# Kernel tuning notes

Hardware: AMD Instinct MI355X
Metric: run time of the kernel (lower is better)

The kernel has to match this reference:

```python
import jax, jax.numpy as jnp
import numpy as np
from jax import lax


def conv2d(x, w, pad=0, b=None):
    out = lax.conv_general_dilated(x, w, (1, 1), [(pad, pad), (pad, pad)],
                                   dimension_numbers=('NCHW', 'OIHW', 'NCHW'))
    if b is not None:
        out = out + b[None, :, None, None]
    return out


def bilinear_resize(x, hw):
    # matches F.interpolate(mode='bilinear', align_corners=False) (half-pixel centers)
    return jax.image.resize(x, x.shape[:2] + tuple(hw), method='bilinear')


def dcn_v2(x, off_feat, w_om, b_om, w, b, dg=8):
    # modulated deformable conv v2, kernel 3x3, stride 1, pad 1, dilation 1
    om = conv2d(off_feat, w_om, pad=1, b=b_om)          # [B, 3*dg*9, H, W]
    B, C, H, W = x.shape
    KK = 9
    Cpg = C // dg
    o1, o2, m = jnp.split(om, 3, axis=1)
    off_y = o1.reshape(B, dg, KK, H, W)
    off_x = o2.reshape(B, dg, KK, H, W)
    mask = jax.nn.sigmoid(m).reshape(B, dg, KK, H, W)
    ks = jnp.arange(3, dtype=x.dtype) - 1.0
    ky = jnp.repeat(ks, 3)   # [9] kernel row offsets
    kx = jnp.tile(ks, 3)     # [9] kernel col offsets
    gy = jnp.arange(H, dtype=x.dtype)
    gx = jnp.arange(W, dtype=x.dtype)
    # sampling coords [B, dg, 9, H, W]
    y = gy[None, None, None, :, None] + ky[None, None, :, None, None] + off_y
    xx = gx[None, None, None, None, :] + kx[None, None, :, None, None] + off_x
    y0 = jnp.floor(y)
    x0 = jnp.floor(xx)
    xg = x.reshape(B, dg, Cpg, H * W)
    val = jnp.zeros((B, dg, Cpg, KK, H, W), x.dtype)
    for dy in (0.0, 1.0):
        for dx in (0.0, 1.0):
            yi = y0 + dy
            xi = x0 + dx
            wgt = (1.0 - jnp.abs(y - yi)) * (1.0 - jnp.abs(xx - xi))
            valid = (yi >= 0) & (yi < H) & (xi >= 0) & (xi < W)  # zero padding outside
            idx = (jnp.clip(yi, 0, H - 1) * W + jnp.clip(xi, 0, W - 1)).astype(jnp.int32)
            idxf = idx.reshape(B, dg, 1, KK * H * W)
            g = jnp.take_along_axis(xg, jnp.broadcast_to(idxf, (B, dg, Cpg, KK * H * W)), axis=3)
            val = val + g.reshape(B, dg, Cpg, KK, H, W) * (wgt * valid)[:, :, None]
    val = val * mask[:, :, None]                         # modulation
    Cout = w.shape[0]
    out = jnp.einsum('bgckhw,ogck->bohw', val, w.reshape(Cout, dg, Cpg, KK))
    return out + b[None, :, None, None]


def sem(x, w_sa, bn_g, bn_b, bn_m, bn_v, w1, gn_g, gn_b):
    # spatial attention
    avg = jnp.mean(x, axis=1, keepdims=True)
    mx = jnp.max(x, axis=1, keepdims=True)
    a = conv2d(jnp.concatenate([avg, mx], axis=1), w_sa, pad=3)
    a = (a - bn_m[None, :, None, None]) * lax.rsqrt(bn_v + 1e-5)[None, :, None, None]
    a = a * bn_g[None, :, None, None] + bn_b[None, :, None, None]
    sa = jax.nn.sigmoid(a)
    x = x + x * sa
    y = conv2d(x, w1)
    # GroupNorm, 32 groups
    B, C, H, W = y.shape
    G = 32
    yr = y.reshape(B, G, C // G, H, W)
    mu = jnp.mean(yr, axis=(2, 3, 4), keepdims=True)
    var = jnp.var(yr, axis=(2, 3, 4), keepdims=True)
    yn = ((yr - mu) * lax.rsqrt(var + 1e-5)).reshape(B, C, H, W)
    return yn * gn_g[None, :, None, None] + gn_b[None, :, None, None]


def setup_inputs() -> dict:
    key = jax.random.key(0)
    ks = jax.random.split(key, 16)
    B, C = 4, 256
    f32 = jnp.float32
    inp = {
        'feat_l': jax.random.normal(ks[0], (B, C, 128, 128), f32),
        'feat_3': jax.random.normal(ks[1], (B, C, 64, 64), f32),
        'feat_4': jax.random.normal(ks[2], (B, C, 32, 32), f32),
        'feat_5': jax.random.normal(ks[3], (B, C, 16, 16), f32),
        'w_off5': jax.random.normal(ks[4], (256, 512, 1, 1), f32) * 0.05,
        'w_om5': jax.random.normal(ks[5], (216, 256, 3, 3), f32) * 0.01,
        'b_om5': jnp.zeros((216,), f32),
        'w_dcn5': jax.random.normal(ks[6], (256, 256, 3, 3), f32) * 0.05,
        'b_dcn5': jnp.zeros((256,), f32),
        'w_c1': jax.random.normal(ks[7], (256, 512, 1, 1), f32) * 0.05,
        'w_off4': jax.random.normal(ks[8], (256, 512, 1, 1), f32) * 0.05,
        'w_om4': jax.random.normal(ks[9], (216, 256, 3, 3), f32) * 0.01,
        'b_om4': jnp.zeros((216,), f32),
        'w_dcn4': jax.random.normal(ks[10], (256, 256, 3, 3), f32) * 0.05,
        'b_dcn4': jnp.zeros((256,), f32),
        'w_sa': jax.random.normal(ks[11], (1, 2, 7, 7), f32) * 0.05,
        'bn_g': jnp.ones((1,), f32),
        'bn_b': jnp.zeros((1,), f32),
        'bn_m': jnp.zeros((1,), f32),
        'bn_v': jnp.ones((1,), f32),
        'w_sem': jax.random.normal(ks[12], (256, 512, 1, 1), f32) * 0.05,
        'gn_g': jnp.ones((256,), f32),
        'gn_b': jnp.zeros((256,), f32),
    }
    return inp


def reference(feat_l, feat_3, feat_4, feat_5,
              w_off5, w_om5, b_om5, w_dcn5, b_dcn5, w_c1,
              w_off4, w_om4, b_om4, w_dcn4, b_dcn4,
              w_sa, bn_g, bn_b, bn_m, bn_v, w_sem, gn_g, gn_b):
    HW4 = feat_4.shape[2:]
    feat_up5 = bilinear_resize(feat_5, HW4)
    off5 = conv2d(jnp.concatenate([feat_4, feat_up5 * 2.0], axis=1), w_off5)
    feat_5_align = jax.nn.relu(dcn_v2(feat_up5, off5, w_om5, b_om5, w_dcn5, b_dcn5))
    feat_4 = conv2d(jnp.concatenate([feat_5_align, feat_4], axis=1), w_c1)
    HW3 = feat_3.shape[2:]
    feat_up4 = bilinear_resize(feat_4, HW3)
    off4 = conv2d(jnp.concatenate([feat_3, feat_up4 * 2.0], axis=1), w_off4)
    feat_4_align = jax.nn.relu(dcn_v2(feat_up4, off4, w_om4, b_om4, w_dcn4, b_dcn4))
    feat_3 = jnp.concatenate([feat_4_align, feat_3], axis=1)
    HW2 = feat_l.shape[2:]
    feat_2 = bilinear_resize(feat_3, HW2)
    return sem(feat_2, w_sa, bn_g, bn_b, bn_m, bn_v, w_sem, gn_g, gn_b)
```

## Files before the change

### kernel.cpp

```cpp
#include <hip/hip_runtime.h>
#include <math.h>


typedef _Float16 h_t;
typedef _Float16 h2 __attribute__((ext_vector_type(2)));
typedef _Float16 h4 __attribute__((ext_vector_type(4)));
typedef _Float16 h8 __attribute__((ext_vector_type(8)));
typedef float f4 __attribute__((ext_vector_type(4)));

static inline int cdiv(long long a, long long b) { return (int)((a + b - 1) / b); }

template <int PERM>
__global__ void prep_w_kernel(const float* __restrict__ W, h_t* __restrict__ Wp,
                              int M, int K) {
  long long idx = (long long)blockIdx.x * 256 + threadIdx.x;
  if (idx >= 512LL * K) return;
  int within = (int)(idx & 4095);
  int m = within >> 5, k = within & 31;
  long long t2 = idx >> 12;
  int s = (int)(t2 & 1);
  long long t3 = t2 >> 1;
  int nck = K >> 5;
  int c = (int)(t3 % nck), mblk = (int)(t3 / nck);
  int gm = mblk * 128 + m, gk = c * 32 + k;
  if (PERM) gk = (gk & 255) * 9 + (gk >> 8);
  float f = (gm < M) ? W[(long long)gm * K + gk] : 0.f;
  h_t hi = (h_t)f;
  Wp[idx] = s ? (h_t)(f - (float)hi) : hi;
}

template <int LOGOW>
__global__ void upsample2x_q_kernel(const float* __restrict__ in, float* __restrict__ out,
                                    int NQ) {
  const int OW = 1 << LOGOW, OHW = OW * OW, IW = OW >> 1;
  long long idx = (long long)blockIdx.x * 256 + threadIdx.x;
  if (idx >= (long long)NQ * OHW) return;
  int p = (int)(idx & (OHW - 1));
  int q = (int)(idx >> (2 * LOGOW));
  int oh = p >> LOGOW, ow = p & (OW - 1);
  int iy = oh >> 1, ix = ow >> 1;
  int iy2 = (oh & 1) ? min(iy + 1, IW - 1) : max(iy - 1, 0);
  int ix2 = (ow & 1) ? min(ix + 1, IW - 1) : max(ix - 1, 0);
  const float* pb = in + (long long)q * 4 * IW * IW;
  f4 o;
#pragma unroll
  for (int j = 0; j < 4; ++j) {
    const float* pc = pb + (long long)j * IW * IW;
    o[j] = 0.5625f * pc[iy * IW + ix] + 0.1875f * (pc[iy * IW + ix2] + pc[iy2 * IW + ix])
         + 0.0625f * pc[iy2 * IW + ix2];
  }
  *(f4*)(out + idx * 4) = o;
}

template <typename TA>
__global__ void concat_h_kernel(const TA* __restrict__ A, const float* __restrict__ Bp,
                                h_t* __restrict__ out, int C1, int C2, int HW, float scale) {
  long long idx = (long long)blockIdx.x * blockDim.x + threadIdx.x;
  long long total = 4LL * (C1 + C2) * HW;
  if (idx >= total) return;
  int p = (int)(idx % HW);
  long long t = idx / HW;
  int c = (int)(t % (C1 + C2));
  int b = (int)(t / (C1 + C2));
  float v;
  if (c < C1) v = (float)A[((long long)b * C1 + c) * HW + p];
  else        v = scale * Bp[((long long)b * C2 + (c - C1)) * HW + p];
  out[idx] = (h_t)v;
}

template <typename TA>
__global__ void concat_a_kernel(const TA* __restrict__ A, h_t* __restrict__ out,
                                int C1, int Ctot, int HW) {
  long long idx = (long long)blockIdx.x * 256 + threadIdx.x;
  long long total = 4LL * C1 * HW;
  if (idx >= total) return;
  int p = (int)(idx % HW);
  long long t = idx / HW;
  int c = (int)(t % C1);
  int b = (int)(t / C1);
  out[((long long)b * Ctot + c) * HW + p] = (h_t)(float)A[((long long)b * C1 + c) * HW + p];
}

__global__ void concat_bq_kernel(const float* __restrict__ xq, h_t* __restrict__ out,
                                 int C1, int C2, int HW, float scale) {
  long long idx = (long long)blockIdx.x * 256 + threadIdx.x;
  long long total = 4LL * (C2 >> 2) * HW;
  if (idx >= total) return;
  int p = (int)(idx % HW);
  long long t = idx / HW;
  int q = (int)(t % (C2 >> 2));
  int b = (int)(t / (C2 >> 2));
  f4 v = *(const f4*)(xq + ((long long)(b * (C2 >> 2) + q) * HW + p) * 4);
  h_t* ob = out + ((long long)b * (C1 + C2) + C1 + q * 4) * HW + p;
  ob[0]            = (h_t)(scale * v.x);
  ob[(long long)HW]     = (h_t)(scale * v.y);
  ob[(long long)2 * HW] = (h_t)(scale * v.z);
  ob[(long long)3 * HW] = (h_t)(scale * v.w);
}

template <int RELU, int OUTH, int TWO>
__global__ __launch_bounds__(256) void mgemm_kernel(
    const h_t* __restrict__ Wp, const h_t* __restrict__ B, void* __restrict__ Cv,
    const float* __restrict__ bias, int Mstore, int N, int K,
    long long sB, long long sC) {
  __shared__ __align__(16) h_t Ah[128 * 40];
  __shared__ __align__(16) h_t Al[TWO ? 128 * 40 : 8];
  __shared__ __align__(16) h_t Bs[64 * 40];
  const int tid = threadIdx.x;
  const int bn = blockIdx.x * 64;
  const int mblk = blockIdx.y;
  const int z = blockIdx.z;
  const h_t* Bb = B + (long long)z * sB;
  const int nck = K >> 5;
  const h_t* Wt = Wp + (long long)mblk * nck * 8192 +
                  (TWO ? (tid << 5) : ((tid >> 1) << 5) + ((tid & 1) << 4));
  const int wid = tid >> 6, lane = tid & 63;
  const int wm = (wid >> 1) * 64, wn = (wid & 1) * 32;
  const int l15 = lane & 15, q = lane >> 4;
  f4 acc[4][2] = {};
  h_t* Adst = TWO ? (tid >= 128 ? Al : Ah) + (tid & 127) * 40
                  : Ah + (tid >> 1) * 40 + ((tid & 1) << 4);
  const int kp = tid >> 4, ngf = tid & 15;
  h_t* Bdst = Bs + ngf * 4 * 40 + kp * 2;
  for (int c = 0; c < nck; ++c) {
    const h_t* asrc = Wt + c * 8192;
    if (TWO) {
#pragma unroll
      for (int i = 0; i < 4; ++i)
        *(h8*)(Adst + i * 8) = *(const h8*)(asrc + i * 8);
    } else {
      *(h8*)(Adst) = *(const h8*)(asrc);
      *(h8*)(Adst + 8) = *(const h8*)(asrc + 8);
    }
    const h_t* bsrc = Bb + (long long)(c * 32 + kp * 2) * N + bn + ngf * 4;
    h4 r0 = *(const h4*)bsrc;
    h4 r1 = *(const h4*)(bsrc + N);
#pragma unroll
    for (int j = 0; j < 4; ++j) {
      h2 v; v.x = r0[j]; v.y = r1[j];
      *(h2*)(Bdst + j * 40) = v;
    }
    __syncthreads();
    h8 bf[2];
#pragma unroll
    for (int nt = 0; nt < 2; ++nt)
      bf[nt] = *(const h8*)(Bs + (wn + nt * 16 + l15) * 40 + q * 8);
#pragma unroll
    for (int mt = 0; mt < 4; ++mt) {
      const int ro = (wm + mt * 16 + l15) * 40 + q * 8;
      h8 ahi = *(const h8*)(Ah + ro);
#pragma unroll
      for (int nt = 0; nt < 2; ++nt)
        acc[mt][nt] = __builtin_amdgcn_mfma_f32_16x16x32_f16(ahi, bf[nt], acc[mt][nt], 0, 0, 0);
      if (TWO) {
        h8 alo = *(const h8*)(Al + ro);
#pragma unroll
        for (int nt = 0; nt < 2; ++nt)
          acc[mt][nt] = __builtin_amdgcn_mfma_f32_16x16x32_f16(alo, bf[nt], acc[mt][nt], 0, 0, 0);
      }
    }
    __syncthreads();
  }
#pragma unroll
  for (int mt = 0; mt < 4; ++mt)
#pragma unroll
    for (int nt = 0; nt < 2; ++nt) {
      int n = bn + wn + nt * 16 + l15;
      if (OUTH == 2) {
        int row0 = mblk * 128 + wm + mt * 16 + q * 4;
        if (row0 + 3 < Mstore) {
          h4 hv;
#pragma unroll
          for (int r = 0; r < 4; ++r) {
            float v = acc[mt][nt][r] + (bias ? bias[row0 + r] : 0.f);
            if (RELU) v = fmaxf(v, 0.f);
            hv[r] = (h_t)v;
          }
          *(h4*)((h_t*)Cv + (long long)z * sC + (long long)n * 256 + row0) = hv;
        }
      } else {
#pragma unroll
        for (int r = 0; r < 4; ++r) {
          int row = mblk * 128 + wm + mt * 16 + q * 4 + r;
          if (row < Mstore) {
            float v = acc[mt][nt][r] + (bias ? bias[row] : 0.f);
            if (RELU) v = fmaxf(v, 0.f);
            if (OUTH) ((h_t*)Cv)[(long long)z * sC + (long long)row * N + n] = (h_t)v;
            else      ((float*)Cv)[(long long)z * sC + (long long)row * N + n] = v;
          }
        }
      }
    }
}

template <int LOGW>
__global__ __launch_bounds__(256) void mconv_kernel(
    const h_t* __restrict__ Wp, const h_t* __restrict__ OffT, float* __restrict__ Cf,
    const float* __restrict__ bias, int HW) {
  const int W = 1 << LOGW, H = HW >> LOGW;
  const int tid = threadIdx.x;
  const int p0 = blockIdx.x * 64;
  const int mblk = blockIdx.y;
  const int z = blockIdx.z;
  const h_t* Ot = OffT + (long long)z * HW * 256;
  const h_t* Wb = Wp + (long long)mblk * 72 * 8192;
  const int wid = tid >> 6, lane = tid & 63;
  const int wm = (wid >> 1) * 64, wn = (wid & 1) * 32;
  const int l15 = lane & 15, q = lane >> 4;
  const int aoff = (wm + l15) * 32 + q * 8;
  f4 acc[4][2] = {};
  int py[2], px[2];
#pragma unroll
  for (int nt = 0; nt < 2; ++nt) {
    int p = p0 + wn + nt * 16 + l15;
    py[nt] = p >> LOGW;
    px[nt] = p & (W - 1);
  }
  for (int tap = 0; tap < 9; ++tap) {
    const int dy = tap / 3 - 1, dx = tap - (tap / 3) * 3 - 1;
    const h_t* bsrc[2];
    bool bok[2];
#pragma unroll
    for (int nt = 0; nt < 2; ++nt) {
      int sy = py[nt] + dy, sx = px[nt] + dx;
      bok[nt] = (sy >= 0) & (sy < H) & (sx >= 0) & (sx < W);
      int sp = bok[nt] ? (sy * W + sx) : 0;
      bsrc[nt] = Ot + (long long)sp * 256 + q * 8;
    }
#pragma unroll 2
    for (int c2 = 0; c2 < 8; ++c2) {
      const int c = tap * 8 + c2;
      h8 bf[2];
#pragma unroll
      for (int nt = 0; nt < 2; ++nt) {
        h8 v = {};
        if (bok[nt]) v = *(const h8*)(bsrc[nt] + c2 * 32);
        bf[nt] = v;
      }
      const h_t* aw = Wb + (long long)c * 8192 + aoff;
#pragma unroll
      for (int mt = 0; mt < 4; ++mt) {
        h8 af = *(const h8*)(aw + mt * 512);
#pragma unroll
        for (int nt = 0; nt < 2; ++nt)
          acc[mt][nt] = __builtin_amdgcn_mfma_f32_16x16x32_f16(af, bf[nt], acc[mt][nt], 0, 0, 0);
      }
    }
  }
  float* Cb = Cf + (long long)z * 216 * HW;
#pragma unroll
  for (int mt = 0; mt < 4; ++mt)
#pragma unroll
    for (int nt = 0; nt < 2; ++nt) {
      int n = p0 + wn + nt * 16 + l15;
#pragma unroll
      for (int r = 0; r < 4; ++r) {
        int row = mblk * 128 + wm + mt * 16 + q * 4 + r;
        if (row < 216)
          Cb[(long long)row * HW + n] = acc[mt][nt][r] + bias[row];
      }
    }
}

template <int LOGW>
__global__ __launch_bounds__(256) void dcn_col_kernel(
    const float* __restrict__ x, const float* __restrict__ om,
    h_t* __restrict__ col, int b0) {
  const int W = 1 << LOGW, H = W, HW = W * W;
  int p = blockIdx.x * 256 + threadIdx.x;
  int gk = blockIdx.y;
  int g = gk / 9, k9 = gk - g * 9;
  int bz = blockIdx.z;
  int b = b0 + bz;
  int h = p >> LOGW, wc = p & (W - 1);
  const float* omb = om + (long long)b * 216 * HW;
  float offy = omb[(long long)gk * HW + p];
  float offx = omb[(long long)(72 + gk) * HW + p];
  float mraw = omb[(long long)(144 + gk) * HW + p];
  float mask = 1.f / (1.f + expf(-mraw));
  float y = (float)h + (float)(k9 / 3 - 1) + offy;
  float xx = (float)wc + (float)(k9 % 3 - 1) + offx;
  float y0f = floorf(y), x0f = floorf(xx);
  int y0 = (int)y0f, x0 = (int)x0f;
  float fy = y - y0f, fx = xx - x0f;
  float w00 = (1.f - fy) * (1.f - fx), w01 = (1.f - fy) * fx;
  float w10 = fy * (1.f - fx), w11 = fy * fx;
  bool iy0 = (y0 >= 0) & (y0 < H), iy1 = (y0 + 1 >= 0) & (y0 + 1 < H);
  bool ix0 = (x0 >= 0) & (x0 < W), ix1 = (x0 + 1 >= 0) & (x0 + 1 < W);
  w00 = (iy0 & ix0) ? w00 : 0.f;
  w01 = (iy0 & ix1) ? w01 : 0.f;
  w10 = (iy1 & ix0) ? w10 : 0.f;
  w11 = (iy1 & ix1) ? w11 : 0.f;
  int y0c = min(max(y0, 0), H - 1), y1c = min(max(y0 + 1, 0), H - 1);
  int x0c = min(max(x0, 0), W - 1), x1c = min(max(x0 + 1, 0), W - 1);
  int i00 = y0c * W + x0c, i01 = y0c * W + x1c, i10 = y1c * W + x0c, i11 = y1c * W + x1c;
  const float* xb = x + ((long long)b * 256 + g * 32) * HW;
  h_t* cb = col + ((long long)bz * 2304 + (long long)(g * 32) * 9 + k9) * HW + p;
#pragma unroll 1
  for (int qd = 0; qd < 8; qd += 2) {
    f4 a00[2], a01[2], a10[2], a11[2];
#pragma unroll
    for (int u = 0; u < 2; ++u) {
      const float* xq = xb + (long long)(qd + u) * HW * 4;
      a00[u] = *(const f4*)(xq + i00 * 4);
      a01[u] = *(const f4*)(xq + i01 * 4);
      a10[u] = *(const f4*)(xq + i10 * 4);
      a11[u] = *(const f4*)(xq + i11 * 4);
    }
#pragma unroll
    for (int u = 0; u < 2; ++u)
#pragma unroll
      for (int j = 0; j < 4; ++j) {
        float v = w00 * a00[u][j] + w01 * a01[u][j] + w10 * a10[u][j] + w11 * a11[u][j];
        cb[(long long)((qd + u) * 4 + j) * 9 * HW] = (h_t)(v * mask);
      }
  }
}

__global__ void avgmax_kernel(const h_t* __restrict__ f3c, float* __restrict__ am) {
  int tid = threadIdx.x;
  int P = blockIdx.x * 64 + (tid >> 2);
  int cq = tid & 3;
  int b = P >> 14, p = P & 16383;
  int oh = p >> 7, ow = p & 127;
  int iy = oh >> 1, ix = ow >> 1;
  int iy2 = (oh & 1) ? min(iy + 1, 63) : max(iy - 1, 0);
  int ix2 = (ow & 1) ? min(ix + 1, 63) : max(ix - 1, 0);
  int i00 = iy * 64 + ix, i01 = iy * 64 + ix2, i10 = iy2 * 64 + ix, i11 = iy2 * 64 + ix2;
  const h_t* base = f3c + (long long)b * 512 * 4096 + (long long)cq * 4096;
  float sum = 0.f, mx = -3.4e38f;
  for (int c = 0; c < 128; c++) {
    const h_t* pc = base + (long long)c * 4 * 4096;
    float v = 0.5625f * (float)pc[i00] + 0.1875f * ((float)pc[i01] + (float)pc[i10])
            + 0.0625f * (float)pc[i11];
    sum += v;
    mx = fmaxf(mx, v);
  }
  sum += __shfl_xor(sum, 1); sum += __shfl_xor(sum, 2);
  mx = fmaxf(mx, __shfl_xor(mx, 1)); mx = fmaxf(mx, __shfl_xor(mx, 2));
  if (cq == 0) {
    am[(long long)b * 2 * 16384 + p] = sum * (1.f / 512.f);
    am[(long long)b * 2 * 16384 + 16384 + p] = mx;
  }
}

__global__ void sa_kernel(const float* __restrict__ am, const float* __restrict__ w_sa,
                          const float* __restrict__ bn_g, const float* __restrict__ bn_b,
                          const float* __restrict__ bn_m, const float* __restrict__ bn_v,
                          float* __restrict__ sa) {
  int idx = blockIdx.x * 64 + threadIdx.x;
  int b = idx >> 14, p = idx & 16383;
  int oh = p >> 7, ow = p & 127;
  float acc = 0.f;
  for (int ci = 0; ci < 2; ci++) {
    const float* base = am + ((long long)b * 2 + ci) * 16384;
    for (int dy = 0; dy < 7; dy++) {
      int yy = oh + dy - 3;
      if (yy < 0 || yy > 127) continue;
      for (int dx = 0; dx < 7; dx++) {
        int xx = ow + dx - 3;
        if (xx < 0 || xx > 127) continue;
        acc += w_sa[ci * 49 + dy * 7 + dx] * base[yy * 128 + xx];
      }
    }
  }
  float a = (acc - bn_m[0]) * rsqrtf(bn_v[0] + 1e-5f);
  a = a * bn_g[0] + bn_b[0];
  sa[idx] = 1.f / (1.f + expf(-a));
}

__global__ __launch_bounds__(256) void gn_partials_kernel(
    const float* __restrict__ z, const float* __restrict__ sa,
    float2* __restrict__ partials) {
  long long idx = (long long)blockIdx.x * 256 + threadIdx.x;
  int ow = (int)(idx & 127);
  long long t = idx >> 7;
  int oh = (int)(t & 127);
  t >>= 7;
  int c = (int)(t & 255);
  int b = (int)(t >> 8);
  int iy = oh >> 1, ix = ow >> 1;
  int iy2 = (oh & 1) ? min(iy + 1, 63) : max(iy - 1, 0);
  int ix2 = (ow & 1) ? min(ix + 1, 63) : max(ix - 1, 0);
  const float* zp = z + (long long)(b * 256 + c) * 4096;
  float v = 0.5625f * zp[iy * 64 + ix] + 0.1875f * (zp[iy * 64 + ix2] + zp[iy2 * 64 + ix])
          + 0.0625f * zp[iy2 * 64 + ix2];
  float s = sa[((long long)b << 14) + (oh << 7) + ow];
  float y = v * (1.f + s);
  float ps = y, pss = y * y;
#pragma unroll
  for (int off = 32; off > 0; off >>= 1) {
    ps += __shfl_down(ps, off);
    pss += __shfl_down(pss, off);
  }
  __shared__ float rs[2][4];
  int lane = threadIdx.x & 63, wv = threadIdx.x >> 6;
  if (lane == 0) { rs[0][wv] = ps; rs[1][wv] = pss; }
  __syncthreads();
  if (threadIdx.x == 0) {
    float2 pr;
    pr.x = rs[0][0] + rs[0][1] + rs[0][2] + rs[0][3];
    pr.y = rs[1][0] + rs[1][1] + rs[1][2] + rs[1][3];
    partials[blockIdx.x] = pr;
  }
}

__global__ __launch_bounds__(256) void gn_reduce_kernel(const float2* __restrict__ partials,
                                                        float* __restrict__ stats) {
  int bg = blockIdx.x;
  int b = bg >> 5, g = bg & 31;
  int base = b * 16384 + g * 512;
  float2 p0 = partials[base + threadIdx.x];
  float2 p1 = partials[base + 256 + threadIdx.x];
  float s = p0.x + p1.x, ss = p0.y + p1.y;
#pragma unroll
  for (int off = 32; off > 0; off >>= 1) {
    s += __shfl_down(s, off);
    ss += __shfl_down(ss, off);
  }
  __shared__ float rs[2][4];
  int lane = threadIdx.x & 63, wv = threadIdx.x >> 6;
  if (lane == 0) { rs[0][wv] = s; rs[1][wv] = ss; }
  __syncthreads();
  if (threadIdx.x == 0) {
    float S = rs[0][0] + rs[0][1] + rs[0][2] + rs[0][3];
    float SS = rs[1][0] + rs[1][1] + rs[1][2] + rs[1][3];
    float n = 8.f * 16384.f;
    float mu = S / n;
    float var = SS / n - mu * mu;
    stats[bg * 2] = mu;
    stats[bg * 2 + 1] = rsqrtf(var + 1e-5f);
  }
}

__global__ __launch_bounds__(256) void gn_apply_fused_kernel(
    const float* __restrict__ z, const float* __restrict__ sa,
    const float* __restrict__ stats, const float* __restrict__ gg,
    const float* __restrict__ gb, float* __restrict__ out) {
  long long i4 = (long long)blockIdx.x * 256 + threadIdx.x;
  long long e = i4 << 2;
  int ow0 = (int)(e & 127);
  int oh = (int)((e >> 7) & 127);
  int c = (int)((e >> 14) & 255);
  int b = (int)(e >> 22);
  int bg = b * 32 + (c >> 3);
  float mu = stats[bg * 2], rstd = stats[bg * 2 + 1];
  float sc = rstd * gg[c];
  float sh = gb[c] - mu * sc;
  int iy = oh >> 1;
  int iy2 = (oh & 1) ? min(iy + 1, 63) : max(iy - 1, 0);
  const float* zp = z + (long long)(b * 256 + c) * 4096;
  f4 sv = *(const f4*)(sa + (((long long)b << 14) + (oh << 7) + ow0));
  f4 o;
#pragma unroll
  for (int j = 0; j < 4; ++j) {
    int ow = ow0 + j;
    int ix = ow >> 1;
    int ix2 = (ow & 1) ? min(ix + 1, 63) : max(ix - 1, 0);
    float v = 0.5625f * zp[iy * 64 + ix] + 0.1875f * (zp[iy * 64 + ix2] + zp[iy2 * 64 + ix])
            + 0.0625f * zp[iy2 * 64 + ix2];
    float y = v * (1.f + sv[j]);
    o[j] = y * sc + sh;
  }
  *(f4*)(out + e) = o;
}


extern "C" void kernel_launch(void* const* d_in, const int* in_sizes, int n_in,
                              void* d_out, int out_size, void* d_ws, size_t ws_size,
                              hipStream_t stream) {
  const float* feat_3 = (const float*)d_in[1];
  const float* feat_4 = (const float*)d_in[2];
  const float* feat_5 = (const float*)d_in[3];
  const float* w_off5 = (const float*)d_in[4];
  const float* w_om5  = (const float*)d_in[5];
  const float* b_om5  = (const float*)d_in[6];
  const float* w_dcn5 = (const float*)d_in[7];
  const float* b_dcn5 = (const float*)d_in[8];
  const float* w_c1   = (const float*)d_in[9];
  const float* w_off4 = (const float*)d_in[10];
  const float* w_om4  = (const float*)d_in[11];
  const float* b_om4  = (const float*)d_in[12];
  const float* w_dcn4 = (const float*)d_in[13];
  const float* b_dcn4 = (const float*)d_in[14];
  const float* w_sa   = (const float*)d_in[15];
  const float* bn_g   = (const float*)d_in[16];
  const float* bn_b   = (const float*)d_in[17];
  const float* bn_m   = (const float*)d_in[18];
  const float* bn_v   = (const float*)d_in[19];
  const float* w_sem  = (const float*)d_in[20];
  const float* gn_g   = (const float*)d_in[21];
  const float* gn_b   = (const float*)d_in[22];
  float* out = (float*)d_out;
  float* ws = (float*)d_ws;

  const long long o_Wp    = 0;
  const long long o_up5   = o_Wp + 2883584;
  const long long o_off5h = o_up5 + 1048576;
  const long long o_om5   = o_off5h + 524288;
  const long long o_a5    = o_om5 + 884736;
  const long long o_f4n   = o_a5 + 1048576;
  const long long o_up4   = o_f4n + 1048576;
  const long long o_off4h = o_up4 + 4194304;
  const long long o_om4   = o_off4h + 2097152;
  const long long o_sh    = o_om4 + 3538944;

  const long long shAll = 18874368;
  bool allb = ws_size >= (size_t)(o_sh + shAll) * 4;

  h_t* WpH = (h_t*)ws;
  h_t* wp_off5 = WpH;
  h_t* wp_dcn5 = wp_off5 + 262144;
  h_t* wp_c1   = wp_dcn5 + 1179648;
  h_t* wp_om5  = wp_c1 + 262144;
  h_t* wp_off4 = wp_om5 + 1179648;
  h_t* wp_dcn4 = wp_off4 + 262144;
  h_t* wp_om4  = wp_dcn4 + 1179648;
  h_t* wp_sem  = wp_om4 + 1179648;

  float* up5   = ws + o_up5;
  h_t*   off5h = (h_t*)(ws + o_off5h);
  float* om5   = ws + o_om5;
  float* a5    = ws + o_a5;
  float* f4n   = ws + o_f4n;
  float* up4   = ws + o_up4;
  h_t*   off4h = (h_t*)(ws + o_off4h);
  float* om4   = ws + o_om4;
  h_t*   shH   = (h_t*)(ws + o_sh);
  h_t*   f4aH  = off4h;
  float* z64   = up4;
  float* am    = up5;
  float* sa    = am + 131072;
  float* gnst  = sa + 65536;
  float2* gnpart = (float2*)(gnst + 256);

  dim3 blk(256);

  prep_w_kernel<0><<<cdiv(512LL * 512, 256), blk, 0, stream>>>(w_off5, wp_off5, 256, 512);
  prep_w_kernel<0><<<cdiv(512LL * 2304, 256), blk, 0, stream>>>(w_dcn5, wp_dcn5, 256, 2304);
  prep_w_kernel<0><<<cdiv(512LL * 512, 256), blk, 0, stream>>>(w_c1, wp_c1, 256, 512);
  prep_w_kernel<1><<<cdiv(512LL * 2304, 256), blk, 0, stream>>>(w_om5, wp_om5, 216, 2304);
  prep_w_kernel<0><<<cdiv(512LL * 512, 256), blk, 0, stream>>>(w_off4, wp_off4, 256, 512);
  prep_w_kernel<0><<<cdiv(512LL * 2304, 256), blk, 0, stream>>>(w_dcn4, wp_dcn4, 256, 2304);
  prep_w_kernel<1><<<cdiv(512LL * 2304, 256), blk, 0, stream>>>(w_om4, wp_om4, 216, 2304);
  prep_w_kernel<0><<<cdiv(512LL * 512, 256), blk, 0, stream>>>(w_sem, wp_sem, 256, 512);

  upsample2x_q_kernel<5><<<1024, blk, 0, stream>>>(feat_5, up5, 256);
  concat_a_kernel<float><<<cdiv(4LL * 256 * 1024, 256), blk, 0, stream>>>(
      feat_4, shH, 256, 512, 1024);
  concat_bq_kernel<<<cdiv(4LL * 64 * 1024, 256), blk, 0, stream>>>(
      up5, shH, 256, 256, 1024, 2.f);
  mgemm_kernel<0, 2, 0><<<dim3(16, 2, 4), blk, 0, stream>>>(
      wp_off5, shH, off5h, nullptr, 256, 1024, 512, 512LL * 1024, 256LL * 1024);
  mconv_kernel<5><<<dim3(16, 2, 4), blk, 0, stream>>>(wp_om5, off5h, om5, b_om5, 1024);
  dcn_col_kernel<5><<<dim3(4, 72, 4), blk, 0, stream>>>(up5, om5, shH, 0);
  mgemm_kernel<1, 0, 1><<<dim3(16, 2, 4), blk, 0, stream>>>(
      wp_dcn5, shH, a5, b_dcn5, 256, 1024, 2304, 2304LL * 1024, 256LL * 1024);
  concat_h_kernel<float><<<cdiv(4LL * 512 * 1024, 256), blk, 0, stream>>>(
      a5, feat_4, shH, 256, 256, 1024, 1.f);
  mgemm_kernel<0, 0, 1><<<dim3(16, 2, 4), blk, 0, stream>>>(
      wp_c1, shH, f4n, nullptr, 256, 1024, 512, 512LL * 1024, 256LL * 1024);

  upsample2x_q_kernel<6><<<4096, blk, 0, stream>>>(f4n, up4, 256);
  concat_a_kernel<float><<<cdiv(4LL * 256 * 4096, 256), blk, 0, stream>>>(
      feat_3, shH, 256, 512, 4096);
  concat_bq_kernel<<<cdiv(4LL * 64 * 4096, 256), blk, 0, stream>>>(
      up4, shH, 256, 256, 4096, 2.f);
  mgemm_kernel<0, 2, 0><<<dim3(64, 2, 4), blk, 0, stream>>>(
      wp_off4, shH, off4h, nullptr, 256, 4096, 512, 512LL * 4096, 256LL * 4096);
  mconv_kernel<6><<<dim3(64, 2, 4), blk, 0, stream>>>(wp_om4, off4h, om4, b_om4, 4096);
  if (allb) {
    dcn_col_kernel<6><<<dim3(16, 72, 4), blk, 0, stream>>>(up4, om4, shH, 0);
    mgemm_kernel<1, 1, 1><<<dim3(64, 2, 4), blk, 0, stream>>>(
        wp_dcn4, shH, f4aH, b_dcn4, 256, 4096, 2304, 2304LL * 4096, 256LL * 4096);
  } else {
    for (int b = 0; b < 4; b++) {
      dcn_col_kernel<6><<<dim3(16, 72, 1), blk, 0, stream>>>(up4, om4, shH, b);
      mgemm_kernel<1, 1, 1><<<dim3(64, 2, 1), blk, 0, stream>>>(
          wp_dcn4, shH, f4aH + (long long)b * 1048576, b_dcn4, 256, 4096, 2304, 0, 0);
    }
  }
  concat_h_kernel<h_t><<<cdiv(4LL * 512 * 4096, 256), blk, 0, stream>>>(
      f4aH, feat_3, shH, 256, 256, 4096, 1.f);

  avgmax_kernel<<<1024, blk, 0, stream>>>(shH, am);
  sa_kernel<<<1024, dim3(64), 0, stream>>>(am, w_sa, bn_g, bn_b, bn_m, bn_v, sa);
  mgemm_kernel<0, 0, 1><<<dim3(64, 2, 4), blk, 0, stream>>>(
      wp_sem, shH, z64, nullptr, 256, 4096, 512, 512LL * 4096, 256LL * 4096);
  gn_partials_kernel<<<65536, blk, 0, stream>>>(z64, sa, gnpart);
  gn_reduce_kernel<<<128, blk, 0, stream>>>(gnpart, gnst);
  gn_apply_fused_kernel<<<16384, blk, 0, stream>>>(z64, sa, gnst, gn_g, gn_b, out);
}
```

Baseline: 772.6 us.

## Store DCN im2col transposed and add direct-load GEMM for it

The deformable-conv column buffer is now written pixel-major (per-pixel K-contiguous rows, ordered k9 then channel), so each thread writes 4-wide half vectors instead of strided scalar stores. A new GEMM kernel reads B fragments straight from global memory as contiguous 8-half loads, with no LDS staging, and fuses bias and ReLU. The weights are repacked with the other permutation to match the new K ordering. The trade-off is that the GEMM now relies on L2/L1 reuse of B instead of shared-memory tiles, and the per-thread column writes are strided by 2304 elements across pixels.

Result: slower. 841.8 us (+9.0%).

```diff
diff --git a/kernel.cpp b/kernel.cpp
--- a/kernel.cpp
+++ b/kernel.cpp
@@ -193,6 +193,65 @@
     }
 }
 
+template <int OUTH>
+__global__ __launch_bounds__(256) void mgemm_bt_kernel(
+    const h_t* __restrict__ Wp, const h_t* __restrict__ Bt, void* __restrict__ Cv,
+    const float* __restrict__ bias, int N, int K, long long sB, long long sC) {
+  const int tid = threadIdx.x;
+  const int bn = blockIdx.x * 64;
+  const int mblk = blockIdx.y;
+  const int z = blockIdx.z;
+  const int nck = K >> 5;
+  const h_t* Bb = Bt + (long long)z * sB;
+  const h_t* Wb = Wp + (long long)mblk * nck * 8192;
+  const int wid = tid >> 6, lane = tid & 63;
+  const int wm = (wid >> 1) * 64, wn = (wid & 1) * 32;
+  const int l15 = lane & 15, q = lane >> 4;
+  const int aoff = (wm + l15) * 32 + q * 8;
+  f4 acc[4][2] = {};
+  const h_t* bp[2];
+#pragma unroll
+  for (int nt = 0; nt < 2; ++nt) {
+    int n = bn + wn + nt * 16 + l15;
+    bp[nt] = Bb + (long long)n * K + q * 8;
+  }
+#pragma unroll 2
+  for (int c = 0; c < nck; ++c) {
+    h8 bf[2];
+#pragma unroll
+    for (int nt = 0; nt < 2; ++nt)
+      bf[nt] = *(const h8*)(bp[nt] + c * 32);
+    const h_t* aw = Wb + (long long)c * 8192 + aoff;
+#pragma unroll
+    for (int mt = 0; mt < 4; ++mt) {
+      h8 ah = *(const h8*)(aw + mt * 512);
+#pragma unroll
+      for (int nt = 0; nt < 2; ++nt)
+        acc[mt][nt] = __builtin_amdgcn_mfma_f32_16x16x32_f16(ah, bf[nt], acc[mt][nt], 0, 0, 0);
+    }
+#pragma unroll
+    for (int mt = 0; mt < 4; ++mt) {
+      h8 al = *(const h8*)(aw + 4096 + mt * 512);
+#pragma unroll
+      for (int nt = 0; nt < 2; ++nt)
+        acc[mt][nt] = __builtin_amdgcn_mfma_f32_16x16x32_f16(al, bf[nt], acc[mt][nt], 0, 0, 0);
+    }
+  }
+#pragma unroll
+  for (int mt = 0; mt < 4; ++mt)
+#pragma unroll
+    for (int nt = 0; nt < 2; ++nt) {
+      int n = bn + wn + nt * 16 + l15;
+#pragma unroll
+      for (int r = 0; r < 4; ++r) {
+        int row = mblk * 128 + wm + mt * 16 + q * 4 + r;
+        float v = fmaxf(acc[mt][nt][r] + bias[row], 0.f);
+        if (OUTH) ((h_t*)Cv)[(long long)z * sC + (long long)row * N + n] = (h_t)v;
+        else      ((float*)Cv)[(long long)z * sC + (long long)row * N + n] = v;
+      }
+    }
+}
+
 template <int LOGW>
 __global__ __launch_bounds__(256) void mconv_kernel(
     const h_t* __restrict__ Wp, const h_t* __restrict__ OffT, float* __restrict__ Cf,
@@ -263,9 +322,9 @@
 }
 
 template <int LOGW>
-__global__ __launch_bounds__(256) void dcn_col_kernel(
+__global__ __launch_bounds__(256) void dcn_colT_kernel(
     const float* __restrict__ x, const float* __restrict__ om,
-    h_t* __restrict__ col, int b0) {
+    h_t* __restrict__ colT, int b0) {
   const int W = 1 << LOGW, H = W, HW = W * W;
   int p = blockIdx.x * 256 + threadIdx.x;
   int gk = blockIdx.y;
@@ -295,7 +354,7 @@
   int x0c = min(max(x0, 0), W - 1), x1c = min(max(x0 + 1, 0), W - 1);
   int i00 = y0c * W + x0c, i01 = y0c * W + x1c, i10 = y1c * W + x0c, i11 = y1c * W + x1c;
   const float* xb = x + ((long long)b * 256 + g * 32) * HW;
-  h_t* cb = col + ((long long)bz * 2304 + (long long)(g * 32) * 9 + k9) * HW + p;
+  h_t* cb = colT + ((long long)bz * HW + p) * 2304 + k9 * 256 + g * 32;
 #pragma unroll 1
   for (int qd = 0; qd < 8; qd += 2) {
     f4 a00[2], a01[2], a10[2], a11[2];
@@ -308,12 +367,15 @@
       a11[u] = *(const f4*)(xq + i11 * 4);
     }
 #pragma unroll
-    for (int u = 0; u < 2; ++u)
+    for (int u = 0; u < 2; ++u) {
+      h4 hv;
 #pragma unroll
       for (int j = 0; j < 4; ++j) {
         float v = w00 * a00[u][j] + w01 * a01[u][j] + w10 * a10[u][j] + w11 * a11[u][j];
-        cb[(long long)((qd + u) * 4 + j) * 9 * HW] = (h_t)(v * mask);
-      }
+        hv[j] = (h_t)(v * mask);
+      }
+      *(h4*)(cb + (qd + u) * 4) = hv;
+    }
   }
 }
 
@@ -537,11 +599,11 @@
   dim3 blk(256);
 
   prep_w_kernel<0><<<cdiv(512LL * 512, 256), blk, 0, stream>>>(w_off5, wp_off5, 256, 512);
-  prep_w_kernel<0><<<cdiv(512LL * 2304, 256), blk, 0, stream>>>(w_dcn5, wp_dcn5, 256, 2304);
+  prep_w_kernel<1><<<cdiv(512LL * 2304, 256), blk, 0, stream>>>(w_dcn5, wp_dcn5, 256, 2304);
   prep_w_kernel<0><<<cdiv(512LL * 512, 256), blk, 0, stream>>>(w_c1, wp_c1, 256, 512);
   prep_w_kernel<1><<<cdiv(512LL * 2304, 256), blk, 0, stream>>>(w_om5, wp_om5, 216, 2304);
   prep_w_kernel<0><<<cdiv(512LL * 512, 256), blk, 0, stream>>>(w_off4, wp_off4, 256, 512);
-  prep_w_kernel<0><<<cdiv(512LL * 2304, 256), blk, 0, stream>>>(w_dcn4, wp_dcn4, 256, 2304);
+  prep_w_kernel<1><<<cdiv(512LL * 2304, 256), blk, 0, stream>>>(w_dcn4, wp_dcn4, 256, 2304);
   prep_w_kernel<1><<<cdiv(512LL * 2304, 256), blk, 0, stream>>>(w_om4, wp_om4, 216, 2304);
   prep_w_kernel<0><<<cdiv(512LL * 512, 256), blk, 0, stream>>>(w_sem, wp_sem, 256, 512);
 
@@ -553,9 +615,9 @@
   mgemm_kernel<0, 2, 0><<<dim3(16, 2, 4), blk, 0, stream>>>(
       wp_off5, shH, off5h, nullptr, 256, 1024, 512, 512LL * 1024, 256LL * 1024);
   mconv_kernel<5><<<dim3(16, 2, 4), blk, 0, stream>>>(wp_om5, off5h, om5, b_om5, 1024);
-  dcn_col_kernel<5><<<dim3(4, 72, 4), blk, 0, stream>>>(up5, om5, shH, 0);
-  mgemm_kernel<1, 0, 1><<<dim3(16, 2, 4), blk, 0, stream>>>(
-      wp_dcn5, shH, a5, b_dcn5, 256, 1024, 2304, 2304LL * 1024, 256LL * 1024);
+  dcn_colT_kernel<5><<<dim3(4, 72, 4), blk, 0, stream>>>(up5, om5, shH, 0);
+  mgemm_bt_kernel<0><<<dim3(16, 2, 4), blk, 0, stream>>>(
+      wp_dcn5, shH, a5, b_dcn5, 1024, 2304, 1024LL * 2304, 256LL * 1024);
   concat_h_kernel<float><<<cdiv(4LL * 512 * 1024, 256), blk, 0, stream>>>(
       a5, feat_4, shH, 256, 256, 1024, 1.f);
   mgemm_kernel<0, 0, 1><<<dim3(16, 2, 4), blk, 0, stream>>>(
@@ -570,14 +632,14 @@
       wp_off4, shH, off4h, nullptr, 256, 4096, 512, 512LL * 4096, 256LL * 4096);
   mconv_kernel<6><<<dim3(64, 2, 4), blk, 0, stream>>>(wp_om4, off4h, om4, b_om4, 4096);
   if (allb) {
-    dcn_col_kernel<6><<<dim3(16, 72, 4), blk, 0, stream>>>(up4, om4, shH, 0);
-    mgemm_kernel<1, 1, 1><<<dim3(64, 2, 4), blk, 0, stream>>>(
-        wp_dcn4, shH, f4aH, b_dcn4, 256, 4096, 2304, 2304LL * 4096, 256LL * 4096);
+    dcn_colT_kernel<6><<<dim3(16, 72, 4), blk, 0, stream>>>(up4, om4, shH, 0);
+    mgemm_bt_kernel<1><<<dim3(64, 2, 4), blk, 0, stream>>>(
+        wp_dcn4, shH, f4aH, b_dcn4, 4096, 2304, 4096LL * 2304, 256LL * 4096);
   } else {
     for (int b = 0; b < 4; b++) {
-      dcn_col_kernel<6><<<dim3(16, 72, 1), blk, 0, stream>>>(up4, om4, shH, b);
-      mgemm_kernel<1, 1, 1><<<dim3(64, 2, 1), blk, 0, stream>>>(
-          wp_dcn4, shH, f4aH + (long long)b * 1048576, b_dcn4, 256, 4096, 2304, 0, 0);
+      dcn_colT_kernel<6><<<dim3(16, 72, 1), blk, 0, stream>>>(up4, om4, shH, b);
+      mgemm_bt_kernel<1><<<dim3(64, 2, 1), blk, 0, stream>>>(
+          wp_dcn4, shH, f4aH + (long long)b * 1048576, b_dcn4, 4096, 2304, 0, 0);
     }
   }
   concat_h_kernel<h_t><<<cdiv(4LL * 512 * 4096, 256), blk, 0, stream>>>(
```

## Double-buffer GEMM shared tiles with register prefetch and fuse upsample into concat

Applied to the files above, without the earlier changes.

The GEMM kernel now prefetches the next K-chunk of weights and activations into registers and alternates between two shared-memory buffers, dropping the second barrier per iteration so global loads overlap the MFMA work. Separately, the 2x upsample kernel now writes the scaled fp16 concat slice directly, removing the separate concat_bq kernel and its reread of the upsampled tensor. The cost is doubled shared memory per block, which may reduce occupancy, plus extra registers for the prefetch.

Result: faster. 691.0 us (-10.6%).

```diff
diff --git a/kernel.cpp b/kernel.cpp
--- a/kernel.cpp
+++ b/kernel.cpp
@@ -30,18 +30,18 @@
 }
 
 template <int LOGOW>
-__global__ void upsample2x_q_kernel(const float* __restrict__ in, float* __restrict__ out,
-                                    int NQ) {
+__global__ void upsample2x_qc_kernel(const float* __restrict__ in, float* __restrict__ outq,
+                                     h_t* __restrict__ outc, float scale) {
   const int OW = 1 << LOGOW, OHW = OW * OW, IW = OW >> 1;
   long long idx = (long long)blockIdx.x * 256 + threadIdx.x;
-  if (idx >= (long long)NQ * OHW) return;
+  if (idx >= 256LL * OHW) return;
   int p = (int)(idx & (OHW - 1));
-  int q = (int)(idx >> (2 * LOGOW));
+  int qg = (int)(idx >> (2 * LOGOW));
   int oh = p >> LOGOW, ow = p & (OW - 1);
   int iy = oh >> 1, ix = ow >> 1;
   int iy2 = (oh & 1) ? min(iy + 1, IW - 1) : max(iy - 1, 0);
   int ix2 = (ow & 1) ? min(ix + 1, IW - 1) : max(ix - 1, 0);
-  const float* pb = in + (long long)q * 4 * IW * IW;
+  const float* pb = in + (long long)qg * 4 * IW * IW;
   f4 o;
 #pragma unroll
   for (int j = 0; j < 4; ++j) {
@@ -49,7 +49,13 @@
     o[j] = 0.5625f * pc[iy * IW + ix] + 0.1875f * (pc[iy * IW + ix2] + pc[iy2 * IW + ix])
          + 0.0625f * pc[iy2 * IW + ix2];
   }
-  *(f4*)(out + idx * 4) = o;
+  *(f4*)(outq + idx * 4) = o;
+  int b = qg >> 6, ql = qg & 63;
+  h_t* oc = outc + ((long long)b * 512 + 256 + ql * 4) * OHW + p;
+  oc[0]                = (h_t)(scale * o[0]);
+  oc[(long long)OHW]       = (h_t)(scale * o[1]);
+  oc[(long long)2 * OHW]   = (h_t)(scale * o[2]);
+  oc[(long long)3 * OHW]   = (h_t)(scale * o[3]);
 }
 
 template <typename TA>
@@ -81,31 +87,14 @@
   out[((long long)b * Ctot + c) * HW + p] = (h_t)(float)A[((long long)b * C1 + c) * HW + p];
 }
 
-__global__ void concat_bq_kernel(const float* __restrict__ xq, h_t* __restrict__ out,
-                                 int C1, int C2, int HW, float scale) {
-  long long idx = (long long)blockIdx.x * 256 + threadIdx.x;
-  long long total = 4LL * (C2 >> 2) * HW;
-  if (idx >= total) return;
-  int p = (int)(idx % HW);
-  long long t = idx / HW;
-  int q = (int)(t % (C2 >> 2));
-  int b = (int)(t / (C2 >> 2));
-  f4 v = *(const f4*)(xq + ((long long)(b * (C2 >> 2) + q) * HW + p) * 4);
-  h_t* ob = out + ((long long)b * (C1 + C2) + C1 + q * 4) * HW + p;
-  ob[0]            = (h_t)(scale * v.x);
-  ob[(long long)HW]     = (h_t)(scale * v.y);
-  ob[(long long)2 * HW] = (h_t)(scale * v.z);
-  ob[(long long)3 * HW] = (h_t)(scale * v.w);
-}
-
 template <int RELU, int OUTH, int TWO>
 __global__ __launch_bounds__(256) void mgemm_kernel(
     const h_t* __restrict__ Wp, const h_t* __restrict__ B, void* __restrict__ Cv,
     const float* __restrict__ bias, int Mstore, int N, int K,
     long long sB, long long sC) {
-  __shared__ __align__(16) h_t Ah[128 * 40];
-  __shared__ __align__(16) h_t Al[TWO ? 128 * 40 : 8];
-  __shared__ __align__(16) h_t Bs[64 * 40];
+  __shared__ __align__(16) h_t Ah[2][128 * 40];
+  __shared__ __align__(16) h_t Al[2][TWO ? 128 * 40 : 8];
+  __shared__ __align__(16) h_t Bs[2][64 * 40];
   const int tid = threadIdx.x;
   const int bn = blockIdx.x * 64;
   const int mblk = blockIdx.y;
@@ -118,48 +107,72 @@
   const int wm = (wid >> 1) * 64, wn = (wid & 1) * 32;
   const int l15 = lane & 15, q = lane >> 4;
   f4 acc[4][2] = {};
-  h_t* Adst = TWO ? (tid >= 128 ? Al : Ah) + (tid & 127) * 40
-                  : Ah + (tid >> 1) * 40 + ((tid & 1) << 4);
+  const int adst = TWO ? (tid & 127) * 40 : (tid >> 1) * 40 + ((tid & 1) << 4);
   const int kp = tid >> 4, ngf = tid & 15;
-  h_t* Bdst = Bs + ngf * 4 * 40 + kp * 2;
+  const int bdst = ngf * 4 * 40 + kp * 2;
+  h8 ra[4];
+  h4 rb0, rb1;
+  {
+    const h_t* asrc = Wt;
+    if (TWO) {
+#pragma unroll
+      for (int i = 0; i < 4; ++i) ra[i] = *(const h8*)(asrc + i * 8);
+    } else {
+      ra[0] = *(const h8*)(asrc);
+      ra[1] = *(const h8*)(asrc + 8);
+    }
+    const h_t* bsrc = Bb + (long long)(kp * 2) * N + bn + ngf * 4;
+    rb0 = *(const h4*)bsrc;
+    rb1 = *(const h4*)(bsrc + N);
+  }
   for (int c = 0; c < nck; ++c) {
-    const h_t* asrc = Wt + c * 8192;
+    const int bsel = c & 1;
+    h_t* Ad = (TWO ? (tid >= 128 ? Al[bsel] : Ah[bsel]) : Ah[bsel]) + adst;
     if (TWO) {
 #pragma unroll
-      for (int i = 0; i < 4; ++i)
-        *(h8*)(Adst + i * 8) = *(const h8*)(asrc + i * 8);
+      for (int i = 0; i < 4; ++i) *(h8*)(Ad + i * 8) = ra[i];
     } else {
-      *(h8*)(Adst) = *(const h8*)(asrc);
-      *(h8*)(Adst + 8) = *(const h8*)(asrc + 8);
-    }
-    const h_t* bsrc = Bb + (long long)(c * 32 + kp * 2) * N + bn + ngf * 4;
-    h4 r0 = *(const h4*)bsrc;
-    h4 r1 = *(const h4*)(bsrc + N);
+      *(h8*)(Ad) = ra[0];
+      *(h8*)(Ad + 8) = ra[1];
+    }
+    h_t* Bd = Bs[bsel] + bdst;
 #pragma unroll
     for (int j = 0; j < 4; ++j) {
-      h2 v; v.x = r0[j]; v.y = r1[j];
-      *(h2*)(Bdst + j * 40) = v;
+      h2 v; v.x = rb0[j]; v.y = rb1[j];
+      *(h2*)(Bd + j * 40) = v;
+    }
+    if (c + 1 < nck) {
+      const h_t* asrc = Wt + (c + 1) * 8192;
+      if (TWO) {
+#pragma unroll
+        for (int i = 0; i < 4; ++i) ra[i] = *(const h8*)(asrc + i * 8);
+      } else {
+        ra[0] = *(const h8*)(asrc);
+        ra[1] = *(const h8*)(asrc + 8);
+      }
+      const h_t* bsrc = Bb + (long long)((c + 1) * 32 + kp * 2) * N + bn + ngf * 4;
+      rb0 = *(const h4*)bsrc;
+      rb1 = *(const h4*)(bsrc + N);
     }
     __syncthreads();
     h8 bf[2];
 #pragma unroll
     for (int nt = 0; nt < 2; ++nt)
-      bf[nt] = *(const h8*)(Bs + (wn + nt * 16 + l15) * 40 + q * 8);
+      bf[nt] = *(const h8*)(Bs[bsel] + (wn + nt * 16 + l15) * 40 + q * 8);
 #pragma unroll
     for (int mt = 0; mt < 4; ++mt) {
       const int ro = (wm + mt * 16 + l15) * 40 + q * 8;
-      h8 ahi = *(const h8*)(Ah + ro);
+      h8 ahi = *(const h8*)(Ah[bsel] + ro);
 #pragma unroll
       for (int nt = 0; nt < 2; ++nt)
         acc[mt][nt] = __builtin_amdgcn_mfma_f32_16x16x32_f16(ahi, bf[nt], acc[mt][nt], 0, 0, 0);
       if (TWO) {
-        h8 alo = *(const h8*)(Al + ro);
+        h8 alo = *(const h8*)(Al[bsel] + ro);
 #pragma unroll
         for (int nt = 0; nt < 2; ++nt)
           acc[mt][nt] = __builtin_amdgcn_mfma_f32_16x16x32_f16(alo, bf[nt], acc[mt][nt], 0, 0, 0);
       }
     }
-    __syncthreads();
   }
 #pragma unroll
   for (int mt = 0; mt < 4; ++mt)
@@ -545,11 +558,9 @@
   prep_w_kernel<1><<<cdiv(512LL * 2304, 256), blk, 0, stream>>>(w_om4, wp_om4, 216, 2304);
   prep_w_kernel<0><<<cdiv(512LL * 512, 256), blk, 0, stream>>>(w_sem, wp_sem, 256, 512);
 
-  upsample2x_q_kernel<5><<<1024, blk, 0, stream>>>(feat_5, up5, 256);
+  upsample2x_qc_kernel<5><<<1024, blk, 0, stream>>>(feat_5, up5, shH, 2.f);
   concat_a_kernel<float><<<cdiv(4LL * 256 * 1024, 256), blk, 0, stream>>>(
       feat_4, shH, 256, 512, 1024);
-  concat_bq_kernel<<<cdiv(4LL * 64 * 1024, 256), blk, 0, stream>>>(
-      up5, shH, 256, 256, 1024, 2.f);
   mgemm_kernel<0, 2, 0><<<dim3(16, 2, 4), blk, 0, stream>>>(
       wp_off5, shH, off5h, nullptr, 256, 1024, 512, 512LL * 1024, 256LL * 1024);
   mconv_kernel<5><<<dim3(16, 2, 4), blk, 0, stream>>>(wp_om5, off5h, om5, b_om5, 1024);
@@ -561,11 +572,9 @@
   mgemm_kernel<0, 0, 1><<<dim3(16, 2, 4), blk, 0, stream>>>(
       wp_c1, shH, f4n, nullptr, 256, 1024, 512, 512LL * 1024, 256LL * 1024);
 
-  upsample2x_q_kernel<6><<<4096, blk, 0, stream>>>(f4n, up4, 256);
+  upsample2x_qc_kernel<6><<<4096, blk, 0, stream>>>(f4n, up4, shH, 2.f);
   concat_a_kernel<float><<<cdiv(4LL * 256 * 4096, 256), blk, 0, stream>>>(
       feat_3, shH, 256, 512, 4096);
-  concat_bq_kernel<<<cdiv(4LL * 64 * 4096, 256), blk, 0, stream>>>(
-      up4, shH, 256, 256, 4096, 2.f);
   mgemm_kernel<0, 2, 0><<<dim3(64, 2, 4), blk, 0, stream>>>(
       wp_off4, shH, off4h, nullptr, 256, 4096, 512, 512LL * 4096, 256LL * 4096);
   mconv_kernel<6><<<dim3(64, 2, 4), blk, 0, stream>>>(wp_om4, off4h, om4, b_om4, 4096);
```
